# Optimization experiments

Hardware: AMD Instinct MI355X
Metric: run time of the kernel (lower is better)

Reference implementation:

```python
import jax, jax.numpy as jnp
import numpy as np

NUM_HEADS = 4
HEAD_DIM = 64
IN_CH = 192
KERNEL_SIZES = (3, 5, 7, 9)  # per-head neighborhood size
NEG_INF = -1e30


def setup_inputs() -> dict:
    key = jax.random.key(0)
    k1, k2, k3 = jax.random.split(key, 3)
    x = jax.random.normal(k1, (8, IN_CH, 96, 96), dtype=jnp.float32)
    # QKV conv: out_channels = head_dim * num_heads * 3 = 768, 3x3, pad 1
    w_qkv = jax.random.normal(k2, (HEAD_DIM * NUM_HEADS * 3, IN_CH, 3, 3), dtype=jnp.float32) * 0.02
    b_qkv = jax.random.normal(k3, (HEAD_DIM * NUM_HEADS * 3,), dtype=jnp.float32) * 0.02
    return {"x": x, "w_qkv": w_qkv, "b_qkv": b_qkv}


def _neighborhood_attention(q, k, v, ksize):
    # q, k, v: [N, H, W, D]; KxK zero-padded neighborhood attention with
    # out-of-bounds positions masked out.
    N, H, W, D = q.shape
    pad = ksize // 2
    kp = jnp.pad(k, ((0, 0), (pad, pad), (pad, pad), (0, 0)))
    vp = jnp.pad(v, ((0, 0), (pad, pad), (pad, pad), (0, 0)))
    scale = 1.0 / np.sqrt(D).astype(np.float32)
    rows = jnp.arange(H)
    cols = jnp.arange(W)
    scores, masks = [], []
    for di in range(ksize):
        for dj in range(ksize):
            k_sh = kp[:, di:di + H, dj:dj + W, :]           # shifted keys
            scores.append(jnp.einsum('nhwd,nhwd->nhw', q, k_sh))
            rv = (rows + di - pad >= 0) & (rows + di - pad < H)   # [H]
            cv = (cols + dj - pad >= 0) & (cols + dj - pad < W)   # [W]
            masks.append(rv[:, None] & cv[None, :])               # [H, W]
    scores = jnp.stack(scores, axis=-1) * scale                   # [N,H,W,K2]
    mask = jnp.stack(masks, axis=-1)[None]                        # [1,H,W,K2]
    scores = jnp.where(mask, scores, NEG_INF)
    attn = jax.nn.softmax(scores, axis=-1)                        # [N,H,W,K2]
    out = jnp.zeros_like(q)
    t = 0
    for di in range(ksize):
        for dj in range(ksize):
            out = out + attn[..., t, None] * vp[:, di:di + H, dj:dj + W, :]
            t += 1
    return out  # [N,H,W,D]


def reference(x, w_qkv, b_qkv):
    # Dense QKV projection (Conv2d, stride 1, padding 1 == SAME for k=3)
    qkv = jax.lax.conv_general_dilated(
        x, w_qkv, window_strides=(1, 1), padding='SAME',
        dimension_numbers=('NCHW', 'OIHW', 'NCHW'))
    qkv = qkv + b_qkv[None, :, None, None]
    # transform_to_nhw1c: NCHW -> NHWC, then split channels into
    # num_heads blocks of 3*head_dim, each split into q, k, v.
    N, C, H, W = qkv.shape
    qkv = jnp.transpose(qkv, (0, 2, 3, 1)).reshape(N, H, W, NUM_HEADS, 3, HEAD_DIM)
    outs = []
    for h, ks in enumerate(KERNEL_SIZES):
        q = qkv[..., h, 0, :]
        k = qkv[..., h, 1, :]
        v = qkv[..., h, 2, :]
        o = _neighborhood_attention(q, k, v, ks)       # [N,H,W,D]
        outs.append(jnp.transpose(o, (0, 3, 1, 2)))    # transform_from_nhw1c -> NCHW
    return jnp.stack(outs, axis=0)  # [num_heads, N, D, H, W]
```

## Files before the change

### kernel.cpp

```cpp
#include <hip/hip_runtime.h>
#include <hip/hip_bf16.h>

#define NH 96
#define NW 96
#define NB 8
#define CIN 192
#define COUT 768
#define PH 98

typedef __attribute__((ext_vector_type(8))) unsigned short ushort8;
typedef __attribute__((ext_vector_type(8))) short bf16x8;
typedef __attribute__((ext_vector_type(4))) float f32x4;

static __device__ __forceinline__ unsigned short f2bf(float f) {
    unsigned int u = __float_as_uint(f);
    return (unsigned short)((u + 0x7fffu + ((u >> 16) & 1u)) >> 16);
}

typedef const __attribute__((address_space(1))) unsigned int gu32;
typedef __attribute__((address_space(3))) unsigned int lu32;
static __device__ __forceinline__ void gload16(const void* g, void* l) {
    __builtin_amdgcn_global_load_lds((gu32*)g, (lu32*)l, 16, 0, 0);
}

__global__ __launch_bounds__(256) void pack_x_kernel(
    const float* __restrict__ x, unsigned short* __restrict__ xp)
{
    __shared__ float tile[32][97];
    int bid = blockIdx.x;
    int ct = bid % 6; int y = (bid / 6) % NH; int n = bid / (6 * NH);
    int tid = threadIdx.x;
    int c0 = ct * 32;
    for (int i = tid; i < 32 * 96; i += 256) {
        int c = i / 96, xx = i % 96;
        tile[c][xx] = x[(((size_t)n * CIN + c0 + c) * NH + y) * NW + xx];
    }
    __syncthreads();
    for (int i = tid; i < 96 * 4; i += 256) {
        int xx = i >> 2, ch = i & 3;
        ushort8 pk;
#pragma unroll
        for (int j = 0; j < 8; ++j) pk[j] = f2bf(tile[ch * 8 + j][xx]);
        *(ushort8*)(xp + ((size_t)(n * PH + y + 1) * PH + xx + 1) * CIN + c0 + ch * 8) = pk;
    }
}

__global__ __launch_bounds__(256) void pack_w_kernel(
    const float* __restrict__ w, unsigned short* __restrict__ bw)
{
    __shared__ float ls[1728];
    int co = blockIdx.x; int tid = threadIdx.x;
    for (int i = tid; i < 1728; i += 256) ls[i] = w[(size_t)co * 1728 + i];
    __syncthreads();
    for (int i = tid; i < 1728; i += 256) {
        int sh = i / 192, ci = i % 192;
        bw[(size_t)co * 1728 + i] = f2bf(ls[ci * 9 + sh]);
    }
}

#define BUFSZ 24576

#define STAGE(S, BUF)                                                          \
    {                                                                          \
        int shift_ = (S) / 6, kk_ = (S) - shift_ * 6;                          \
        int aO_ = ((shift_ / 3) * PH + (shift_ % 3)) * CIN + kk_ * 32;         \
        int bO_ = (S) * 32;                                                    \
        gload16(srcA[0] + aO_, dstA[0] + (BUF));                               \
        gload16(srcA[1] + aO_, dstA[1] + (BUF));                               \
        _Pragma("unroll")                                                      \
        for (int i_ = 0; i_ < 4; ++i_)                                         \
            gload16(srcB[i_] + bO_, dstB[i_] + (BUF));                         \
    }

#define COMPUTE(CUR)                                                           \
    {                                                                          \
        bf16x8 af[8], bf[4];                                                   \
        _Pragma("unroll")                                                      \
        for (int m_ = 0; m_ < 8; ++m_)                                         \
            af[m_] = *(const bf16x8*)(smem + (CUR) + aoff[m_]);                \
        _Pragma("unroll")                                                      \
        for (int n_ = 0; n_ < 4; ++n_)                                         \
            bf[n_] = *(const bf16x8*)(smem + (CUR) + boff[n_]);                \
        __builtin_amdgcn_s_setprio(1);                                         \
        _Pragma("unroll")                                                      \
        for (int m_ = 0; m_ < 8; ++m_)                                         \
            _Pragma("unroll")                                                  \
            for (int n_ = 0; n_ < 4; ++n_)                                     \
                acc[m_][n_] = __builtin_amdgcn_mfma_f32_16x16x32_bf16(         \
                    af[m_], bf[n_], acc[m_][n_], 0, 0, 0);                     \
        __builtin_amdgcn_s_setprio(0);                                         \
    }

__global__ __launch_bounds__(256, 2) void conv_gemm_kernel(
    const unsigned short* __restrict__ xp, const unsigned short* __restrict__ bw,
    const float* __restrict__ bias, unsigned short* __restrict__ qkq,
    unsigned short* __restrict__ vt)
{
    __shared__ __align__(16) char smem[3 * BUFSZ];
    int bid = (blockIdx.x & 7) * 216 + (blockIdx.x >> 3);
    int brow = (bid / 3) * 128, bcol = (bid % 3) * 256;
    int tid = threadIdx.x, lane = tid & 63, wn = tid >> 6;

    const unsigned short* srcA[2];
    const unsigned short* srcB[4];
    char* dstA[2];
    char* dstB[4];
#pragma unroll
    for (int i = 0; i < 2; ++i) {
        int s = i * 256 + tid;
        int row = s >> 2, c = s & 3;
        int p = brow + row;
        int n = p / 9216; int rem = p - n * 9216;
        int y = rem / 96; int xx = rem - y * 96;
        int csw = (c ^ ((row >> 1) & 3)) << 3;
        srcA[i] = xp + ((size_t)(n * PH + y) * PH + xx) * CIN + csw;
        dstA[i] = smem + (i * 256 + (tid & ~63)) * 16;
    }
#pragma unroll
    for (int i = 0; i < 4; ++i) {
        int s = i * 256 + tid;
        int row = s >> 2, c = s & 3;
        int csw = (c ^ ((row >> 1) & 3)) << 3;
        srcB[i] = bw + (size_t)(bcol + row) * 1728 + csw;
        dstB[i] = smem + 8192 + (i * 256 + (tid & ~63)) * 16;
    }

    int aoff[8], boff[4];
#pragma unroll
    for (int m = 0; m < 8; ++m) {
        int rowA = m * 16 + (lane & 15);
        aoff[m] = rowA * 64 + (((lane >> 4) ^ ((rowA >> 1) & 3)) << 4);
    }
#pragma unroll
    for (int n = 0; n < 4; ++n) {
        int colB = wn * 64 + n * 16 + (lane & 15);
        boff[n] = 8192 + colB * 64 + (((lane >> 4) ^ ((colB >> 1) & 3)) << 4);
    }

    STAGE(0, 0);
    STAGE(1, BUFSZ);

    f32x4 acc[8][4] = {};

    for (int t = 0; t < 52; ++t) {
        asm volatile("s_waitcnt vmcnt(6)" ::: "memory");
        __builtin_amdgcn_s_barrier();
        STAGE(t + 2, ((t + 2) % 3) * BUFSZ);
        __builtin_amdgcn_sched_barrier(0);
        COMPUTE((t % 3) * BUFSZ);
    }
    asm volatile("s_waitcnt vmcnt(6)" ::: "memory");
    __builtin_amdgcn_s_barrier();
    COMPUTE((52 % 3) * BUFSZ);
    asm volatile("s_waitcnt vmcnt(0)" ::: "memory");
    __builtin_amdgcn_s_barrier();
    COMPUTE((53 % 3) * BUFSZ);

    __syncthreads();
    unsigned short* sc = (unsigned short*)smem;
    float bn[4];
#pragma unroll
    for (int n = 0; n < 4; ++n)
        bn[n] = bias[bcol + wn * 64 + n * 16 + (lane & 15)];
#pragma unroll
    for (int m = 0; m < 8; ++m)
#pragma unroll
        for (int n = 0; n < 4; ++n) {
            int col = wn * 64 + n * 16 + (lane & 15);
            int cabs = bcol + col;
            float scale = ((cabs % 192) < 64) ? 0.125f : 1.0f;
#pragma unroll
            for (int j = 0; j < 4; ++j) {
                int row = m * 16 + (lane >> 4) * 4 + j;
                sc[row * 256 + (col ^ ((row & 7) << 3))] =
                    f2bf((acc[m][n][j] + bn[n]) * scale);
            }
        }
    __syncthreads();
#pragma unroll
    for (int i = 0; i < 16; ++i) {
        int idx = i * 256 + tid;
        int row = idx >> 5, ch = idx & 31;
        int c0 = bcol + ch * 8;
        int r192 = c0 % 192;
        if (r192 < 128) {
            ushort8 pk = *(const ushort8*)(sc + row * 256 + ((ch * 8) ^ ((row & 7) << 3)));
            *(ushort8*)(qkq + (size_t)(brow + row) * 512 + (c0 / 192) * 128 + r192) = pk;
        }
    }
    int nblk = brow / 9216;
    int prem = brow - nblk * 9216;
#pragma unroll
    for (int h = 0; h < 4; ++h) {
        int lc = h * 192 + 128 - bcol;
        if (lc < 0 || lc > 192) continue;
        unsigned short* vth = vt + (size_t)h * 4718592;
#pragma unroll
        for (int it = 0; it < 4; ++it) {
            int i = it * 256 + tid;
            int d = i & 63, pxb = i >> 6;
            ushort8 pk;
#pragma unroll
            for (int j = 0; j < 8; ++j) {
                int px = pxb * 8 + j;
                pk[j] = sc[px * 256 + ((lc + d) ^ ((px & 7) << 3))];
            }
            *(ushort8*)(vth + ((size_t)(nblk * 64 + d)) * 9216 + prem + pxb * 8) = pk;
        }
    }
}

#define SLAB 24576
template<int KS>
static __device__ __forceinline__ void na_body(
    const unsigned short* __restrict__ qkq, const unsigned short* __restrict__ vt,
    float* __restrict__ out, int head, int bid, char* nsm)
{
    constexpr int PAD = KS / 2;
    int yp = bid % 48, n = bid / 48;
    int y0 = yp * 2;
    int tid = threadIdx.x;
    int wv = tid >> 6, lane = tid & 63;
    int g = lane >> 4, pix = lane & 15;
    int x0 = wv * 16;
    int x = x0 + pix;
    int W = x0 - 8;

    size_t qb0 = ((size_t)((n * 96 + y0) * 96 + x)) * 512 + (size_t)head * 128;
    size_t qb1 = qb0 + 96 * 512;
    bf16x8 qa0 = *(const bf16x8*)(qkq + qb0 + g * 8);
    bf16x8 qa1 = *(const bf16x8*)(qkq + qb0 + 32 + g * 8);
    bf16x8 qc0 = *(const bf16x8*)(qkq + qb1 + g * 8);
    bf16x8 qc1 = *(const bf16x8*)(qkq + qb1 + 32 + g * 8);
    asm volatile("s_waitcnt vmcnt(0)" ::: "memory");

    const size_t hoff = (size_t)head * 128 + 64;
#define STAGEKV(DI, BUF)                                                       \
    {                                                                          \
        int iy_ = min(max(y0 + (DI) - PAD, 0), 95);                            \
        size_t rb_ = ((size_t)((n * 96 + iy_) * 96)) * 512 + hoff;             \
        _Pragma("unroll")                                                      \
        for (int i_ = 0; i_ < 2; ++i_) {                                       \
            int ch_ = i_ * 384 + tid;                                          \
            int xx_ = ch_ >> 3, c8_ = (ch_ & 7) ^ (xx_ & 7);                   \
            gload16(qkq + rb_ + (size_t)xx_ * 512 + c8_ * 8,                   \
                    nsm + (BUF) * SLAB + (i_ * 384 + (tid & ~63)) * 16);       \
        }                                                                      \
        _Pragma("unroll")                                                      \
        for (int i_ = 0; i_ < 2; ++i_) {                                       \
            int ch_ = i_ * 384 + tid;                                          \
            int d_ = ch_ / 12, c_ = ch_ % 12;                                  \
            int cs_ = c_ ^ ((d_ >> 1) & 3);                                    \
            gload16(vt + (((size_t)(n * 64 + d_) * 96 + iy_)) * 96 + cs_ * 8,  \
                    nsm + (BUF) * SLAB + 12288 + (i_ * 384 + (tid & ~63)) * 16); \
        }                                                                      \
    }

    STAGEKV(0, 0);
    STAGEKV(1, 1);

    float l0 = 0.f, l1 = 0.f;
    f32x4 O0[4] = {}, O1[4] = {};
    int addrA = ((2 * (g & 1)) * 16 + pix) * 4;
    int addrB = addrA + 64;
    bool kthi = (g >> 1) != 0;
    int cxg = min(max(2 * wv - 1 + g, 0), 11);
    int vbase = 12288 + pix * 192 + ((cxg ^ ((pix >> 1) & 3)) << 4);

#define ROWCOMP(QF0, QF1, L, O)                                                \
    {                                                                          \
        unsigned int w0[2], w1[2];                                             \
        _Pragma("unroll")                                                      \
        for (int kt = 0; kt < 2; ++kt) {                                       \
            f32x4 tt = {};                                                     \
            tt = __builtin_amdgcn_mfma_f32_16x16x32_bf16(kf0[kt], QF0, tt, 0, 0, 0); \
            tt = __builtin_amdgcn_mfma_f32_16x16x32_bf16(kf1[kt], QF1, tt, 0, 0, 0); \
            float p[4];                                                        \
            _Pragma("unroll")                                                  \
            for (int r = 0; r < 4; ++r) {                                      \
                int kix = W + kt * 16 + g * 4 + r;                             \
                bool valid = ((unsigned)(kix - x + PAD) <= (unsigned)(2 * PAD)) && \
                             ((unsigned)kix < 96u);                            \
                p[r] = valid ? __expf(tt[r]) : 0.f;                            \
            }                                                                  \
            L += (p[0] + p[1]) + (p[2] + p[3]);                                \
            asm("v_cvt_pk_bf16_f32 %0, %1, %2" : "=v"(w0[kt]) : "v"(p[0]), "v"(p[1])); \
            asm("v_cvt_pk_bf16_f32 %0, %1, %2" : "=v"(w1[kt]) : "v"(p[2]), "v"(p[3])); \
        }                                                                      \
        int a0 = __builtin_amdgcn_ds_bpermute(addrA, (int)w0[0]);              \
        int b0 = __builtin_amdgcn_ds_bpermute(addrA, (int)w0[1]);              \
        int a1 = __builtin_amdgcn_ds_bpermute(addrA, (int)w1[0]);              \
        int b1 = __builtin_amdgcn_ds_bpermute(addrA, (int)w1[1]);              \
        int a2 = __builtin_amdgcn_ds_bpermute(addrB, (int)w0[0]);              \
        int b2 = __builtin_amdgcn_ds_bpermute(addrB, (int)w0[1]);              \
        int a3 = __builtin_amdgcn_ds_bpermute(addrB, (int)w1[0]);              \
        int b3 = __builtin_amdgcn_ds_bpermute(addrB, (int)w1[1]);              \
        union { int u[4]; bf16x8 v; } pa;                                      \
        pa.u[0] = kthi ? b0 : a0;                                              \
        pa.u[1] = kthi ? b1 : a1;                                              \
        pa.u[2] = kthi ? b2 : a2;                                              \
        pa.u[3] = kthi ? b3 : a3;                                              \
        _Pragma("unroll")                                                      \
        for (int dc = 0; dc < 4; ++dc)                                         \
            O[dc] = __builtin_amdgcn_mfma_f32_16x16x32_bf16(pa.v, vf[dc], O[dc], 0, 0, 0); \
    }

#pragma unroll
    for (int di = 0; di <= KS; ++di) {
        if (di < KS) asm volatile("s_waitcnt vmcnt(4)" ::: "memory");
        else         asm volatile("s_waitcnt vmcnt(0)" ::: "memory");
        __builtin_amdgcn_s_barrier();
        __builtin_amdgcn_sched_barrier(0);
        if (di + 2 <= KS) STAGEKV(di + 2, (di + 2) % 3);
        int iy = y0 + di - PAD;
        if (iy < 0 || iy >= 96) continue;
        const char* kb = nsm + (di % 3) * SLAB;

        bf16x8 kf0[2], kf1[2];
#pragma unroll
        for (int kt = 0; kt < 2; ++kt) {
            int kix_l = W + kt * 16 + pix;
            int ixc = min(max(kix_l, 0), 95);
            const char* kr = kb + ixc * 128;
            kf0[kt] = *(const bf16x8*)(kr + ((g ^ (ixc & 7)) << 4));
            kf1[kt] = *(const bf16x8*)(kr + (((4 + g) ^ (ixc & 7)) << 4));
        }
        bf16x8 vf[4];
#pragma unroll
        for (int dc = 0; dc < 4; ++dc)
            vf[dc] = *(const bf16x8*)(kb + dc * 3072 + vbase);

        if (di < KS)  ROWCOMP(qa0, qa1, l0, O0);
        if (di >= 1)  ROWCOMP(qc0, qc1, l1, O1);
    }

    l0 += __shfl_xor(l0, 16, 64); l0 += __shfl_xor(l0, 32, 64);
    l1 += __shfl_xor(l1, 16, 64); l1 += __shfl_xor(l1, 32, 64);
    float li0 = 1.0f / l0, li1 = 1.0f / l1;
    float lj0[4], lj1[4];
#pragma unroll
    for (int j = 0; j < 4; ++j) {
        lj0[j] = __uint_as_float((unsigned)__builtin_amdgcn_ds_bpermute(
            (4 * g + j) * 4, (int)__float_as_uint(li0)));
        lj1[j] = __uint_as_float((unsigned)__builtin_amdgcn_ds_bpermute(
            (4 * g + j) * 4, (int)__float_as_uint(li1)));
    }
    __syncthreads();
    float (*sO2)[64][97] = (float(*)[64][97])nsm;
#pragma unroll
    for (int dc = 0; dc < 4; ++dc)
#pragma unroll
        for (int j = 0; j < 4; ++j) {
            sO2[0][dc * 16 + pix][x0 + g * 4 + j] = O0[dc][j] * lj0[j];
            sO2[1][dc * 16 + pix][x0 + g * 4 + j] = O1[dc][j] * lj1[j];
        }
    __syncthreads();
    for (int i = tid; i < 3072; i += 384) {
        int r = i >> 11;
        int rem = i - r * 1536;
        r = i / 1536; rem = i - r * 1536;
        int d = rem / 24, xq = rem % 24;
        float4 v4 = { sO2[r][d][xq * 4], sO2[r][d][xq * 4 + 1],
                      sO2[r][d][xq * 4 + 2], sO2[r][d][xq * 4 + 3] };
        *(float4*)(out + ((size_t)(head * 8 + n) * 64 + d) * 9216
                   + (y0 + r) * 96 + xq * 4) = v4;
    }
}

__global__ __launch_bounds__(384, 2) void na_mfma_all(
    const unsigned short* __restrict__ qkq, const unsigned short* __restrict__ vt,
    float* __restrict__ out)
{
    __shared__ __align__(16) char nsm[3 * SLAB];
    int head = blockIdx.x & 3;
    int bid = blockIdx.x >> 2;
    switch (head) {
        case 0: na_body<3>(qkq, vt,               out, 0, bid, nsm); break;
        case 1: na_body<5>(qkq, vt + 4718592,     out, 1, bid, nsm); break;
        case 2: na_body<7>(qkq, vt + 2 * 4718592, out, 2, bid, nsm); break;
        default: na_body<9>(qkq, vt + 3 * 4718592, out, 3, bid, nsm); break;
    }
}

extern "C" void kernel_launch(void* const* d_in, const int* in_sizes, int n_in,
                              void* d_out, int out_size, void* d_ws, size_t ws_size,
                              hipStream_t stream) {
    const float* x  = (const float*)d_in[0];
    const float* w  = (const float*)d_in[1];
    const float* b  = (const float*)d_in[2];
    float* out = (float*)d_out;

    unsigned short* qkq  = (unsigned short*)d_ws;
    unsigned short* vt   = (unsigned short*)((char*)d_ws + 75497472);
    unsigned short* xpad = (unsigned short*)((char*)d_ws + 113246208);
    unsigned short* bw   = (unsigned short*)((char*)d_ws + 142749696);

    hipMemsetAsync(xpad, 0, 29503488, stream);
    pack_x_kernel<<<NB * NH * 6, 256, 0, stream>>>(x, xpad);
    pack_w_kernel<<<COUT, 256, 0, stream>>>(w, bw);
    conv_gemm_kernel<<<1728, 256, 0, stream>>>(xpad, bw, b, qkq, vt);

    na_mfma_all<<<4 * 384, 384, 0, stream>>>(qkq, vt, out);
}
```

Baseline: 329.6 us.

## Shrink conv GEMM LDS to double buffer for three blocks per CU

```diff
diff --git a/kernel.cpp b/kernel.cpp
--- a/kernel.cpp
+++ b/kernel.cpp
@@ -91,12 +91,12 @@
         __builtin_amdgcn_s_setprio(0);                                         \
     }
 
-__global__ __launch_bounds__(256, 2) void conv_gemm_kernel(
+__global__ __launch_bounds__(256, 3) void conv_gemm_kernel(
     const unsigned short* __restrict__ xp, const unsigned short* __restrict__ bw,
     const float* __restrict__ bias, unsigned short* __restrict__ qkq,
     unsigned short* __restrict__ vt)
 {
-    __shared__ __align__(16) char smem[3 * BUFSZ];
+    __shared__ __align__(16) char smem[2 * BUFSZ];
     int bid = (blockIdx.x & 7) * 216 + (blockIdx.x >> 3);
     int brow = (bid / 3) * 128, bcol = (bid % 3) * 256;
     int tid = threadIdx.x, lane = tid & 63, wn = tid >> 6;
@@ -138,23 +138,17 @@
     }
 
     STAGE(0, 0);
-    STAGE(1, BUFSZ);
 
     f32x4 acc[8][4] = {};
 
-    for (int t = 0; t < 52; ++t) {
-        asm volatile("s_waitcnt vmcnt(6)" ::: "memory");
+    for (int t = 0; t < 54; ++t) {
+        asm volatile("s_waitcnt vmcnt(0)" ::: "memory");
         __builtin_amdgcn_s_barrier();
-        STAGE(t + 2, ((t + 2) % 3) * BUFSZ);
         __builtin_amdgcn_sched_barrier(0);
-        COMPUTE((t % 3) * BUFSZ);
-    }
-    asm volatile("s_waitcnt vmcnt(6)" ::: "memory");
-    __builtin_amdgcn_s_barrier();
-    COMPUTE((52 % 3) * BUFSZ);
-    asm volatile("s_waitcnt vmcnt(0)" ::: "memory");
-    __builtin_amdgcn_s_barrier();
-    COMPUTE((53 % 3) * BUFSZ);
+        if (t < 53) STAGE(t + 1, ((t + 1) & 1) * BUFSZ);
+        __builtin_amdgcn_sched_barrier(0);
+        COMPUTE((t & 1) * BUFSZ);
+    }
 
     __syncthreads();
     unsigned short* sc = (unsigned short*)smem;
@@ -162,51 +156,59 @@
 #pragma unroll
     for (int n = 0; n < 4; ++n)
         bn[n] = bias[bcol + wn * 64 + n * 16 + (lane & 15)];
-#pragma unroll
-    for (int m = 0; m < 8; ++m)
-#pragma unroll
-        for (int n = 0; n < 4; ++n) {
-            int col = wn * 64 + n * 16 + (lane & 15);
-            int cabs = bcol + col;
-            float scale = ((cabs % 192) < 64) ? 0.125f : 1.0f;
-#pragma unroll
-            for (int j = 0; j < 4; ++j) {
-                int row = m * 16 + (lane >> 4) * 4 + j;
-                sc[row * 256 + (col ^ ((row & 7) << 3))] =
-                    f2bf((acc[m][n][j] + bn[n]) * scale);
+    int nblk = brow / 9216;
+    int prem = brow - nblk * 9216;
+#pragma unroll
+    for (int p = 0; p < 2; ++p) {
+#pragma unroll
+        for (int mm = 0; mm < 4; ++mm) {
+            int m = p * 4 + mm;
+#pragma unroll
+            for (int n = 0; n < 4; ++n) {
+                int col = wn * 64 + n * 16 + (lane & 15);
+                int cabs = bcol + col;
+                float scale = ((cabs % 192) < 64) ? 0.125f : 1.0f;
+#pragma unroll
+                for (int j = 0; j < 4; ++j) {
+                    int row = mm * 16 + (lane >> 4) * 4 + j;
+                    sc[row * 256 + (col ^ ((row & 7) << 3))] =
+                        f2bf((acc[m][n][j] + bn[n]) * scale);
+                }
             }
         }
-    __syncthreads();
-#pragma unroll
-    for (int i = 0; i < 16; ++i) {
-        int idx = i * 256 + tid;
-        int row = idx >> 5, ch = idx & 31;
-        int c0 = bcol + ch * 8;
-        int r192 = c0 % 192;
-        if (r192 < 128) {
-            ushort8 pk = *(const ushort8*)(sc + row * 256 + ((ch * 8) ^ ((row & 7) << 3)));
-            *(ushort8*)(qkq + (size_t)(brow + row) * 512 + (c0 / 192) * 128 + r192) = pk;
+        __syncthreads();
+#pragma unroll
+        for (int i = 0; i < 8; ++i) {
+            int idx = i * 256 + tid;
+            int row = idx >> 5, ch = idx & 31;
+            int c0 = bcol + ch * 8;
+            int r192 = c0 % 192;
+            if (r192 < 128) {
+                ushort8 pk = *(const ushort8*)(sc + row * 256 + ((ch * 8) ^ ((row & 7) << 3)));
+                *(ushort8*)(qkq + (size_t)(brow + p * 64 + row) * 512
+                            + (c0 / 192) * 128 + r192) = pk;
+            }
         }
-    }
-    int nblk = brow / 9216;
-    int prem = brow - nblk * 9216;
-#pragma unroll
-    for (int h = 0; h < 4; ++h) {
-        int lc = h * 192 + 128 - bcol;
-        if (lc < 0 || lc > 192) continue;
-        unsigned short* vth = vt + (size_t)h * 4718592;
-#pragma unroll
-        for (int it = 0; it < 4; ++it) {
-            int i = it * 256 + tid;
-            int d = i & 63, pxb = i >> 6;
-            ushort8 pk;
-#pragma unroll
-            for (int j = 0; j < 8; ++j) {
-                int px = pxb * 8 + j;
-                pk[j] = sc[px * 256 + ((lc + d) ^ ((px & 7) << 3))];
+#pragma unroll
+        for (int h = 0; h < 4; ++h) {
+            int lc = h * 192 + 128 - bcol;
+            if (lc < 0 || lc > 192) continue;
+            unsigned short* vth = vt + (size_t)h * 4718592;
+#pragma unroll
+            for (int it = 0; it < 2; ++it) {
+                int i = it * 256 + tid;
+                int d = i & 63, pxb = i >> 6;
+                ushort8 pk;
+#pragma unroll
+                for (int j = 0; j < 8; ++j) {
+                    int px = pxb * 8 + j;
+                    pk[j] = sc[px * 256 + ((lc + d) ^ ((px & 7) << 3))];
+                }
+                *(ushort8*)(vth + ((size_t)(nblk * 64 + d)) * 9216
+                            + prem + p * 64 + pxb * 8) = pk;
             }
-            *(ushort8*)(vth + ((size_t)(nblk * 64 + d)) * 9216 + prem + pxb * 8) = pk;
         }
+        __syncthreads();
     }
 }
 
@@ -356,9 +358,8 @@
         }
     __syncthreads();
     for (int i = tid; i < 3072; i += 384) {
-        int r = i >> 11;
+        int r = i / 1536;
         int rem = i - r * 1536;
-        r = i / 1536; rem = i - r * 1536;
         int d = rem / 24, xq = rem % 24;
         float4 v4 = { sO2[r][d][xq * 4], sO2[r][d][xq * 4 + 1],
                       sO2[r][d][xq * 4 + 2], sO2[r][d][xq * 4 + 3] };
```

After: 729.6 us. 121% more time.

## Enlarge conv GEMM tile to 256x256 with 8 waves and K=64 double buffering

Applied to the files above, without the earlier changes.

```diff
diff --git a/kernel.cpp b/kernel.cpp
--- a/kernel.cpp
+++ b/kernel.cpp
@@ -58,103 +58,103 @@
     }
 }
 
-#define BUFSZ 24576
-
-#define STAGE(S, BUF)                                                          \
-    {                                                                          \
-        int shift_ = (S) / 6, kk_ = (S) - shift_ * 6;                          \
-        int aO_ = ((shift_ / 3) * PH + (shift_ % 3)) * CIN + kk_ * 32;         \
-        int bO_ = (S) * 32;                                                    \
-        gload16(srcA[0] + aO_, dstA[0] + (BUF));                               \
-        gload16(srcA[1] + aO_, dstA[1] + (BUF));                               \
-        _Pragma("unroll")                                                      \
-        for (int i_ = 0; i_ < 4; ++i_)                                         \
-            gload16(srcB[i_] + bO_, dstB[i_] + (BUF));                         \
-    }
-
-#define COMPUTE(CUR)                                                           \
-    {                                                                          \
-        bf16x8 af[8], bf[4];                                                   \
-        _Pragma("unroll")                                                      \
-        for (int m_ = 0; m_ < 8; ++m_)                                         \
-            af[m_] = *(const bf16x8*)(smem + (CUR) + aoff[m_]);                \
-        _Pragma("unroll")                                                      \
-        for (int n_ = 0; n_ < 4; ++n_)                                         \
-            bf[n_] = *(const bf16x8*)(smem + (CUR) + boff[n_]);                \
-        __builtin_amdgcn_s_setprio(1);                                         \
-        _Pragma("unroll")                                                      \
-        for (int m_ = 0; m_ < 8; ++m_)                                         \
-            _Pragma("unroll")                                                  \
-            for (int n_ = 0; n_ < 4; ++n_)                                     \
-                acc[m_][n_] = __builtin_amdgcn_mfma_f32_16x16x32_bf16(         \
-                    af[m_], bf[n_], acc[m_][n_], 0, 0, 0);                     \
-        __builtin_amdgcn_s_setprio(0);                                         \
-    }
-
-__global__ __launch_bounds__(256, 2) void conv_gemm_kernel(
+__global__ __launch_bounds__(512) void conv_gemm_kernel(
     const unsigned short* __restrict__ xp, const unsigned short* __restrict__ bw,
     const float* __restrict__ bias, unsigned short* __restrict__ qkq,
     unsigned short* __restrict__ vt)
 {
-    __shared__ __align__(16) char smem[3 * BUFSZ];
-    int bid = (blockIdx.x & 7) * 216 + (blockIdx.x >> 3);
-    int brow = (bid / 3) * 128, bcol = (bid % 3) * 256;
-    int tid = threadIdx.x, lane = tid & 63, wn = tid >> 6;
-
-    const unsigned short* srcA[2];
-    const unsigned short* srcB[4];
-    char* dstA[2];
-    char* dstB[4];
-#pragma unroll
-    for (int i = 0; i < 2; ++i) {
-        int s = i * 256 + tid;
-        int row = s >> 2, c = s & 3;
-        int p = brow + row;
-        int n = p / 9216; int rem = p - n * 9216;
-        int y = rem / 96; int xx = rem - y * 96;
-        int csw = (c ^ ((row >> 1) & 3)) << 3;
-        srcA[i] = xp + ((size_t)(n * PH + y) * PH + xx) * CIN + csw;
-        dstA[i] = smem + (i * 256 + (tid & ~63)) * 16;
-    }
-#pragma unroll
-    for (int i = 0; i < 4; ++i) {
-        int s = i * 256 + tid;
-        int row = s >> 2, c = s & 3;
-        int csw = (c ^ ((row >> 1) & 3)) << 3;
-        srcB[i] = bw + (size_t)(bcol + row) * 1728 + csw;
-        dstB[i] = smem + 8192 + (i * 256 + (tid & ~63)) * 16;
-    }
-
-    int aoff[8], boff[4];
-#pragma unroll
-    for (int m = 0; m < 8; ++m) {
-        int rowA = m * 16 + (lane & 15);
-        aoff[m] = rowA * 64 + (((lane >> 4) ^ ((rowA >> 1) & 3)) << 4);
-    }
-#pragma unroll
-    for (int n = 0; n < 4; ++n) {
-        int colB = wn * 64 + n * 16 + (lane & 15);
-        boff[n] = 8192 + colB * 64 + (((lane >> 4) ^ ((colB >> 1) & 3)) << 4);
-    }
-
-    STAGE(0, 0);
-    STAGE(1, BUFSZ);
+    __shared__ __align__(16) char smem[131072];
+    int bid = (blockIdx.x & 7) * 108 + (blockIdx.x >> 3);
+    int brow = (bid / 3) * 256, bcol = (bid % 3) * 256;
+    int tid = threadIdx.x, lane = tid & 63;
+    int wid = tid >> 6, wm = wid >> 2, wn = wid & 3;
+    int g = lane >> 4;
+
+    const unsigned short* srcA[2][2];
+    const unsigned short* srcB[2][2];
+#pragma unroll
+    for (int h = 0; h < 2; ++h)
+#pragma unroll
+        for (int i = 0; i < 2; ++i) {
+            int s = i * 512 + tid;
+            int rl = s >> 3, c = s & 7;
+            int csw = (c ^ (rl & 7)) << 3;
+            int p = brow + h * 128 + rl;
+            int n = p / 9216; int rem = p - n * 9216;
+            int y = rem / 96; int xx = rem - y * 96;
+            srcA[h][i] = xp + ((size_t)(n * PH + y) * PH + xx) * CIN + csw;
+            srcB[h][i] = bw + (size_t)(bcol + h * 128 + rl) * 1728 + csw;
+        }
+    int dsto[2];
+#pragma unroll
+    for (int i = 0; i < 2; ++i) dsto[i] = (i * 512 + (tid & ~63)) * 16;
+
+#define STAGEU(T, U, BUF)                                                      \
+    {                                                                          \
+        int shift_ = (T) / 3, kk_ = (T) % 3;                                   \
+        if ((U) < 2) {                                                         \
+            int aO_ = ((shift_ / 3) * PH + (shift_ % 3)) * CIN + kk_ * 64;     \
+            _Pragma("unroll")                                                  \
+            for (int i_ = 0; i_ < 2; ++i_)                                     \
+                gload16(srcA[(U)][i_] + aO_,                                   \
+                        smem + (BUF) + (U) * 16384 + dsto[i_]);                \
+        } else {                                                               \
+            int bO_ = (T) * 64;                                                \
+            _Pragma("unroll")                                                  \
+            for (int i_ = 0; i_ < 2; ++i_)                                     \
+                gload16(srcB[(U) - 2][i_] + bO_,                               \
+                        smem + (BUF) + 32768 + ((U) - 2) * 16384 + dsto[i_]);  \
+        }                                                                      \
+    }
+
+    int arow[8], brow_[4], xof[2];
+#pragma unroll
+    for (int m = 0; m < 8; ++m)
+        arow[m] = (wm * 128 + m * 16 + (lane & 15)) * 128;
+#pragma unroll
+    for (int n = 0; n < 4; ++n)
+        brow_[n] = 32768 + (wn * 64 + n * 16 + (lane & 15)) * 128;
+#pragma unroll
+    for (int kk = 0; kk < 2; ++kk)
+        xof[kk] = ((kk * 4 + g) ^ (lane & 7)) << 4;
+
+    STAGEU(0, 0, 0); STAGEU(0, 1, 0); STAGEU(0, 2, 0); STAGEU(0, 3, 0);
 
     f32x4 acc[8][4] = {};
 
-    for (int t = 0; t < 52; ++t) {
-        asm volatile("s_waitcnt vmcnt(6)" ::: "memory");
+    for (int t = 0; t < 27; ++t) {
+        asm volatile("s_waitcnt vmcnt(0)" ::: "memory");
         __builtin_amdgcn_s_barrier();
-        STAGE(t + 2, ((t + 2) % 3) * BUFSZ);
         __builtin_amdgcn_sched_barrier(0);
-        COMPUTE((t % 3) * BUFSZ);
-    }
-    asm volatile("s_waitcnt vmcnt(6)" ::: "memory");
-    __builtin_amdgcn_s_barrier();
-    COMPUTE((52 % 3) * BUFSZ);
-    asm volatile("s_waitcnt vmcnt(0)" ::: "memory");
-    __builtin_amdgcn_s_barrier();
-    COMPUTE((53 % 3) * BUFSZ);
+        const int cur = (t & 1) << 16;
+        const int nxt = cur ^ 65536;
+        bf16x8 bf[4][2];
+#pragma unroll
+        for (int n = 0; n < 4; ++n)
+#pragma unroll
+            for (int kk = 0; kk < 2; ++kk)
+                bf[n][kk] = *(const bf16x8*)(smem + cur + brow_[n] + xof[kk]);
+#pragma unroll
+        for (int p = 0; p < 4; ++p) {
+            if (t < 26) STAGEU(t + 1, p, nxt);
+            bf16x8 af[2][2];
+#pragma unroll
+            for (int mm = 0; mm < 2; ++mm)
+#pragma unroll
+                for (int kk = 0; kk < 2; ++kk)
+                    af[mm][kk] = *(const bf16x8*)(smem + cur + arow[2 * p + mm] + xof[kk]);
+            __builtin_amdgcn_s_setprio(1);
+#pragma unroll
+            for (int mm = 0; mm < 2; ++mm)
+#pragma unroll
+                for (int n = 0; n < 4; ++n)
+#pragma unroll
+                    for (int kk = 0; kk < 2; ++kk)
+                        acc[2 * p + mm][n] = __builtin_amdgcn_mfma_f32_16x16x32_bf16(
+                            af[mm][kk], bf[n][kk], acc[2 * p + mm][n], 0, 0, 0);
+            __builtin_amdgcn_s_setprio(0);
+        }
+    }
 
     __syncthreads();
     unsigned short* sc = (unsigned short*)smem;
@@ -171,7 +171,7 @@
             float scale = ((cabs % 192) < 64) ? 0.125f : 1.0f;
 #pragma unroll
             for (int j = 0; j < 4; ++j) {
-                int row = m * 16 + (lane >> 4) * 4 + j;
+                int row = wm * 128 + m * 16 + (lane >> 4) * 4 + j;
                 sc[row * 256 + (col ^ ((row & 7) << 3))] =
                     f2bf((acc[m][n][j] + bn[n]) * scale);
             }
@@ -179,7 +179,7 @@
     __syncthreads();
 #pragma unroll
     for (int i = 0; i < 16; ++i) {
-        int idx = i * 256 + tid;
+        int idx = i * 512 + tid;
         int row = idx >> 5, ch = idx & 31;
         int c0 = bcol + ch * 8;
         int r192 = c0 % 192;
@@ -197,7 +197,7 @@
         unsigned short* vth = vt + (size_t)h * 4718592;
 #pragma unroll
         for (int it = 0; it < 4; ++it) {
-            int i = it * 256 + tid;
+            int i = it * 512 + tid;
             int d = i & 63, pxb = i >> 6;
             ushort8 pk;
 #pragma unroll
@@ -356,9 +356,8 @@
         }
     __syncthreads();
     for (int i = tid; i < 3072; i += 384) {
-        int r = i >> 11;
+        int r = i / 1536;
         int rem = i - r * 1536;
-        r = i / 1536; rem = i - r * 1536;
         int d = rem / 24, xq = rem % 24;
         float4 v4 = { sO2[r][d][xq * 4], sO2[r][d][xq * 4 + 1],
                       sO2[r][d][xq * 4 + 2], sO2[r][d][xq * 4 + 3] };
@@ -398,7 +397,7 @@
     hipMemsetAsync(xpad, 0, 29503488, stream);
     pack_x_kernel<<<NB * NH * 6, 256, 0, stream>>>(x, xpad);
     pack_w_kernel<<<COUT, 256, 0, stream>>>(w, bw);
-    conv_gemm_kernel<<<1728, 256, 0, stream>>>(xpad, bw, b, qkq, vt);
+    conv_gemm_kernel<<<864, 512, 0, stream>>>(xpad, bw, b, qkq, vt);
 
     na_mfma_all<<<4 * 384, 384, 0, stream>>>(qkq, vt, out);
 }
```

Result: faster. 321.7 us (-2.4%).
